# Kernel tuning notes

Hardware: AMD Instinct MI355X
Metric: run time of the kernel (lower is better)

Reference implementation:

```python
import jax, jax.numpy as jnp
import numpy as np

C = 384          # hardcoded input dim in Head
H = 6            # num_heads
D = 64           # head_size (H*D == C)

def setup_inputs() -> dict:
    key = jax.random.key(0)
    ks = jax.random.split(key, 6)
    x = jax.random.normal(ks[0], (4, 2048, C), dtype=jnp.float32)
    # per-head projection weights stacked: [H, C, D]
    s = 1.0 / np.sqrt(C)
    Wq = jax.random.uniform(ks[1], (H, C, D), minval=-s, maxval=s, dtype=jnp.float32)
    Wk = jax.random.uniform(ks[2], (H, C, D), minval=-s, maxval=s, dtype=jnp.float32)
    Wv = jax.random.uniform(ks[3], (H, C, D), minval=-s, maxval=s, dtype=jnp.float32)
    sp = 1.0 / np.sqrt(H * D)
    Wo = jax.random.uniform(ks[4], (H * D, H * D), minval=-sp, maxval=sp, dtype=jnp.float32)
    bo = jax.random.uniform(ks[5], (H * D,), minval=-sp, maxval=sp, dtype=jnp.float32)
    return {"x": x, "Wq": Wq, "Wk": Wk, "Wv": Wv, "Wo": Wo, "bo": bo}

def reference(x, Wq, Wk, Wv, Wo, bo):
    B, T, _ = x.shape
    # per-head projections (batched over heads instead of a Python loop)
    q = jnp.einsum('btc,hcd->bhtd', x, Wq)
    k = jnp.einsum('btc,hcd->bhtd', x, Wk)
    v = jnp.einsum('btc,hcd->bhtd', x, Wv)
    scale = 1.0 / jnp.sqrt(jnp.asarray(D, dtype=x.dtype))
    scores = jnp.einsum('bhtd,bhsd->bhts', q, k) * scale  # [B,H,T,T]
    attn = jax.nn.softmax(scores, axis=-1)                # no causal mask in source
    out = jnp.einsum('bhts,bhsd->bhtd', attn, v)          # [B,H,T,D]
    # concat heads: [B,T,H*D] (head order matches torch.cat over heads)
    out = out.transpose(0, 2, 1, 3).reshape(B, T, H * D)
    return out @ Wo + bo
```

## Files before the change

### kernel.cpp

```cpp
#include <hip/hip_runtime.h>

typedef unsigned short u16;
typedef float  f32x4 __attribute__((ext_vector_type(4)));
typedef short  s16x8 __attribute__((ext_vector_type(8)));
typedef unsigned int u32x2 __attribute__((ext_vector_type(2)));
typedef unsigned int u32x4 __attribute__((ext_vector_type(4)));

union U8 { u32x4 u; u32x2 u2[2]; s16x8 s; unsigned int uw[4]; };

__device__ __forceinline__ u16 f2bs(float f) {
    union { float f; unsigned int u; } x; x.f = f;
    return (u16)((x.u + 0x7FFFu + ((x.u >> 16) & 1u)) >> 16);
}

__device__ __forceinline__ unsigned int cvtpk(float a, float b) {
    unsigned int r;
    asm("v_cvt_pk_bf16_f32 %0, %1, %2" : "=v"(r) : "v"(a), "v"(b));
    return r;
}

#if __has_builtin(__builtin_amdgcn_exp2f)
#define EXP2(v) __builtin_amdgcn_exp2f(v)
#else
#define EXP2(v) exp2f(v)
#endif

__device__ __forceinline__ f32x4 mfma16(s16x8 a, s16x8 b, f32x4 c) {
    return __builtin_amdgcn_mfma_f32_16x16x32_bf16(a, b, c, 0, 0, 0);
}

typedef __attribute__((address_space(3))) unsigned int lds_u32;
typedef const __attribute__((address_space(1))) unsigned int glb_u32;
__device__ __forceinline__ void gl16(const u16* g, u16* l) {
    __builtin_amdgcn_global_load_lds((glb_u32*)g, (lds_u32*)l, 16, 0, 0);
}

__global__ __launch_bounds__(256) void pack_w2(const float* __restrict__ Wq,
                                               const float* __restrict__ Wk,
                                               const float* __restrict__ Wv,
                                               const float* __restrict__ Wo,
                                               u16* __restrict__ Wt) {
    __shared__ float tile[64][65];
    const int bid = blockIdx.x, tid = threadIdx.x;
    const float* src; u16* dst; int src_ld, sr0, sc0;
    if (bid < 108) {
        int tensor = bid / 36, rem = bid % 36, h = rem / 6, ct = rem % 6;
        const float* W = (tensor == 0) ? Wq : (tensor == 1) ? Wk : Wv;
        src = W + h * 24576; src_ld = 64; sr0 = ct * 64; sc0 = 0;
        dst = Wt + tensor * 147456 + h * 24576;
    } else {
        int rem = bid - 108, et = rem / 6, ft = rem % 6;
        src = Wo; src_ld = 384; sr0 = ft * 64; sc0 = et * 64;
        dst = Wt + 3 * 147456;
    }
    const int r = tid >> 2, cb = (tid & 3) * 16;
    const float* sp = src + (size_t)(sr0 + r) * src_ld + sc0 + cb;
    #pragma unroll
    for (int j = 0; j < 4; ++j)
        *(f32x4*)&tile[r][cb + j * 4] = *(const f32x4*)(sp + j * 4);
    __syncthreads();
    struct alignas(16) OV { u16 v[16]; } ov;
    #pragma unroll
    for (int j = 0; j < 16; ++j) ov.v[j] = f2bs(tile[cb + j][r]);
    u16* dp = dst + (size_t)(sc0 + r) * 384 + sr0 + cb;
    *(u32x4*)dp       = *(u32x4*)&ov.v[0];
    *(u32x4*)(dp + 8) = *(u32x4*)&ov.v[8];
}

__global__ __launch_bounds__(256) void convert_x(const float* __restrict__ x, u16* __restrict__ xb) {
    const int i = (blockIdx.x * 256 + threadIdx.x) * 8;
    f32x4 a = *(const f32x4*)(x + i);
    f32x4 b = *(const f32x4*)(x + i + 4);
    U8 o;
    #pragma unroll
    for (int j = 0; j < 4; ++j) { o.s[j] = (short)f2bs(a[j]); o.s[4 + j] = (short)f2bs(b[j]); }
    *(u32x4*)(xb + i) = o.u;
}

__global__ __launch_bounds__(256) void proj2(const u16* __restrict__ xb,
                                             const u16* __restrict__ Wt,
                                             u16* __restrict__ Qb,
                                             u16* __restrict__ Kb,
                                             u16* __restrict__ Vb) {
    __shared__ u16 As[2][128 * 32];
    __shared__ u16 Bs[2][128 * 32];
    const int tid = threadIdx.x, w = tid >> 6, lane = tid & 63;
    const int lr = lane & 15, lg = lane >> 4;
    const int wr = w >> 1, wc = w & 1;
    const int mt = blockIdx.x, nt = blockIdx.y;
    const int m0 = mt * 128, n0 = nt * 128;

    const int c0 = w * 2 * 64 + lane;
    const int ar0 = c0 >> 2, acc0 = c0 & 3;
    const int c1 = c0 + 64;
    const int ar1 = c1 >> 2, acc1 = c1 & 3;
    const u16* gA0 = xb + (size_t)(m0 + ar0) * 384 + acc0 * 8;
    const u16* gA1 = xb + (size_t)(m0 + ar1) * 384 + acc1 * 8;
    const u16* gB0 = Wt + (size_t)(n0 + ar0) * 384 + acc0 * 8;
    const u16* gB1 = Wt + (size_t)(n0 + ar1) * 384 + acc1 * 8;

    f32x4 acc[4][4];
    #pragma unroll
    for (int i = 0; i < 4; ++i)
        #pragma unroll
        for (int j = 0; j < 4; ++j) acc[i][j] = f32x4{0.f, 0.f, 0.f, 0.f};

    gl16(gA0, &As[0][(w * 2 + 0) * 512]);
    gl16(gA1, &As[0][(w * 2 + 1) * 512]);
    gl16(gB0, &Bs[0][(w * 2 + 0) * 512]);
    gl16(gB1, &Bs[0][(w * 2 + 1) * 512]);
    __syncthreads();

    for (int kt = 0; kt < 12; ++kt) {
        const int buf = kt & 1;
        if (kt < 11) {
            const int ko = (kt + 1) * 32;
            gl16(gA0 + ko, &As[buf ^ 1][(w * 2 + 0) * 512]);
            gl16(gA1 + ko, &As[buf ^ 1][(w * 2 + 1) * 512]);
            gl16(gB0 + ko, &Bs[buf ^ 1][(w * 2 + 0) * 512]);
            gl16(gB1 + ko, &Bs[buf ^ 1][(w * 2 + 1) * 512]);
        }
        U8 af[4], bf[4];
        #pragma unroll
        for (int f = 0; f < 4; ++f) {
            af[f].u = *(const u32x4*)&As[buf][(wr * 64 + f * 16 + lr) * 32 + lg * 8];
            bf[f].u = *(const u32x4*)&Bs[buf][(wc * 64 + f * 16 + lr) * 32 + lg * 8];
        }
        #pragma unroll
        for (int mf = 0; mf < 4; ++mf)
            #pragma unroll
            for (int nf = 0; nf < 4; ++nf)
                acc[mf][nf] = mfma16(af[mf].s, bf[nf].s, acc[mf][nf]);
        __syncthreads();
    }

    const int tensor = nt / 3;
    u16* dst = (tensor == 0) ? Qb : (tensor == 1) ? Kb : Vb;
    const float scl = (tensor == 0) ? 0.18033688011112042f : 1.0f;
    const int head_base = (nt % 3) * 2 + wc;
    #pragma unroll
    for (int mf = 0; mf < 4; ++mf)
        #pragma unroll
        for (int nf = 0; nf < 4; ++nf)
            #pragma unroll
            for (int r = 0; r < 4; ++r) {
                int m = m0 + wr * 64 + mf * 16 + lg * 4 + r;
                int b = m >> 11, t = m & 2047;
                int d = nf * 16 + lr;
                dst[((size_t)(b * 6 + head_base) * 2048 + t) * 64 + d] = f2bs(acc[mf][nf][r] * scl);
            }
}

__global__ __launch_bounds__(256) void transpose_v(const u16* __restrict__ Vb,
                                                   u16* __restrict__ Vt) {
    __shared__ u16 tile[64][72];
    const int bh = blockIdx.y, t0 = blockIdx.x * 64;
    const int tid = threadIdx.x;
    const int r = tid >> 2, c0 = (tid & 3) * 16;
    const u16* src = Vb + ((size_t)bh * 2048 + t0 + r) * 64 + c0;
    u32x4 a  = *(const u32x4*)(src);
    u32x4 b2 = *(const u32x4*)(src + 8);
    *(u32x4*)&tile[r][c0]     = a;
    *(u32x4*)&tile[r][c0 + 8] = b2;
    __syncthreads();
    struct alignas(16) OutV { u16 v[16]; } ov;
    #pragma unroll
    for (int j = 0; j < 16; ++j) ov.v[j] = tile[c0 + j][r];
    u16* dst = Vt + ((size_t)bh * 64 + r) * 2048 + t0 + c0;
    *(u32x4*)dst       = *(u32x4*)&ov.v[0];
    *(u32x4*)(dst + 8) = *(u32x4*)&ov.v[8];
}

__global__ __launch_bounds__(256) void attn3(const u16* __restrict__ Qb,
                                             const u16* __restrict__ Kb,
                                             const u16* __restrict__ Vt,
                                             u16* __restrict__ AO) {
    __shared__ char smem[32768];
    const int tid = threadIdx.x, w = tid >> 6, lane = tid & 63;
    const int lr = lane & 15, lg = lane >> 4;
    const int qt = blockIdx.x, bh = blockIdx.y;
    const int b = bh / 6, h = bh - b * 6;
    const int qbase = qt * 64 + w * 16;

    const u16* qp = Qb + ((size_t)bh * 2048 + qbase + lr) * 64 + lg * 8;
    U8 bq0, bq1;
    bq0.u = *(const u32x4*)qp;
    bq1.u = *(const u32x4*)(qp + 32);

    const int srow = lane >> 3;
    const int slot = lane & 7;
    const int chunk = slot ^ srow;
    const u16* kg0 = Kb + (size_t)bh * 2048 * 64 + (size_t)(w * 16 + srow) * 64 + chunk * 8;
    const u16* kg1 = kg0 + 8 * 64;
    const u16* vg0 = Vt + (size_t)bh * 64 * 2048 + (size_t)(w * 16 + srow) * 2048 + chunk * 8;
    const u16* vg1 = vg0 + 8 * 2048;

    const int rx = lr & 7;
    const int kOffA = lr * 128 + ((lg ^ rx) * 16);
    const int kOffB = lr * 128 + (((4 + lg) ^ rx) * 16);
    const int vRow = lr * 128 + (lg & 1) * 8;
    const int vC = lg >> 1;

    f32x4 acc[4];
    #pragma unroll
    for (int i = 0; i < 4; ++i) acc[i] = f32x4{0.f, 0.f, 0.f, 0.f};
    float rsum = 0.f;

    gl16(kg0, (u16*)(smem + w * 2048));
    gl16(kg1, (u16*)(smem + w * 2048 + 1024));
    gl16(vg0, (u16*)(smem + 8192 + w * 2048));
    gl16(vg1, (u16*)(smem + 8192 + w * 2048 + 1024));
    kg0 += 4096; kg1 += 4096; vg0 += 64; vg1 += 64;
    __syncthreads();

    for (int it = 0; it < 32; ++it) {
        const int buf = it & 1;
        const char* kbase = smem + buf * 16384;
        const char* vbase = kbase + 8192;

        if (it < 31) {
            char* nb = smem + (buf ^ 1) * 16384;
            gl16(kg0, (u16*)(nb + w * 2048));
            gl16(kg1, (u16*)(nb + w * 2048 + 1024));
            gl16(vg0, (u16*)(nb + 8192 + w * 2048));
            gl16(vg1, (u16*)(nb + 8192 + w * 2048 + 1024));
            kg0 += 4096; kg1 += 4096; vg0 += 64; vg1 += 64;
        }

        float p[16];
        const f32x4 z{0.f, 0.f, 0.f, 0.f};
        #pragma unroll
        for (int t = 0; t < 4; ++t) {
            U8 ak0, ak1;
            ak0.u = *(const u32x4*)(kbase + t * 2048 + kOffA);
            ak1.u = *(const u32x4*)(kbase + t * 2048 + kOffB);
            f32x4 s = mfma16(ak0.s, bq0.s, z);
            s = mfma16(ak1.s, bq1.s, s);
            #pragma unroll
            for (int r = 0; r < 4; ++r) p[t * 4 + r] = EXP2(s[r]);
        }
        #pragma unroll
        for (int i = 0; i < 16; ++i) rsum += p[i];

        U8 pa0, pa1;
        #pragma unroll
        for (int i = 0; i < 4; ++i) {
            pa0.uw[i] = cvtpk(p[2 * i],     p[2 * i + 1]);
            pa1.uw[i] = cvtpk(p[8 + 2 * i], p[9 + 2 * i]);
        }

        #pragma unroll
        for (int dt = 0; dt < 4; ++dt) {
            const char* vr = vbase + dt * 2048 + vRow;
            U8 bv0, bv1;
            bv0.u2[0] = *(const u32x2*)(vr + (((0 + vC) ^ rx) << 4));
            bv0.u2[1] = *(const u32x2*)(vr + (((2 + vC) ^ rx) << 4));
            bv1.u2[0] = *(const u32x2*)(vr + (((4 + vC) ^ rx) << 4));
            bv1.u2[1] = *(const u32x2*)(vr + (((6 + vC) ^ rx) << 4));
            acc[dt] = mfma16(pa0.s, bv0.s, acc[dt]);
            acc[dt] = mfma16(pa1.s, bv1.s, acc[dt]);
        }
        __syncthreads();
    }

    rsum += __shfl_xor(rsum, 16, 64);
    rsum += __shfl_xor(rsum, 32, 64);

    const size_t aobase = ((size_t)b * 2048 + qbase) * 384 + h * 64;
    #pragma unroll
    for (int r = 0; r < 4; ++r) {
        float inv = 1.0f / __shfl(rsum, lg * 4 + r, 64);
        #pragma unroll
        for (int dt = 0; dt < 4; ++dt)
            AO[aobase + (size_t)(lg * 4 + r) * 384 + dt * 16 + lr] = f2bs(acc[dt][r] * inv);
    }
}

__global__ __launch_bounds__(256) void outproj2(const u16* __restrict__ AO,
                                                const u16* __restrict__ Wot,
                                                const float* __restrict__ bo,
                                                float* __restrict__ out) {
    __shared__ u16 As[2][64 * 32];
    __shared__ u16 Bs[2][64 * 32];
    const int tid = threadIdx.x, w = tid >> 6, lane = tid & 63;
    const int lr = lane & 15, lg = lane >> 4;
    const int wr = w >> 1, wc = w & 1;
    const int mt = blockIdx.x, nt = blockIdx.y;
    const int m0 = mt * 64, n0 = nt * 64;

    const int c0 = w * 64 + lane;
    const int ar0 = c0 >> 2, cc0 = c0 & 3;
    const u16* gA = AO  + (size_t)(m0 + ar0) * 384 + cc0 * 8;
    const u16* gB = Wot + (size_t)(n0 + ar0) * 384 + cc0 * 8;

    f32x4 acc[2][2];
    #pragma unroll
    for (int i = 0; i < 2; ++i)
        #pragma unroll
        for (int j = 0; j < 2; ++j) acc[i][j] = f32x4{0.f, 0.f, 0.f, 0.f};

    gl16(gA, &As[0][w * 512]);
    gl16(gB, &Bs[0][w * 512]);
    __syncthreads();

    for (int kt = 0; kt < 12; ++kt) {
        const int buf = kt & 1;
        if (kt < 11) {
            const int ko = (kt + 1) * 32;
            gl16(gA + ko, &As[buf ^ 1][w * 512]);
            gl16(gB + ko, &Bs[buf ^ 1][w * 512]);
        }
        U8 af[2], bf[2];
        #pragma unroll
        for (int f = 0; f < 2; ++f) {
            af[f].u = *(const u32x4*)&As[buf][(wr * 32 + f * 16 + lr) * 32 + lg * 8];
            bf[f].u = *(const u32x4*)&Bs[buf][(wc * 32 + f * 16 + lr) * 32 + lg * 8];
        }
        #pragma unroll
        for (int mf = 0; mf < 2; ++mf)
            #pragma unroll
            for (int nf = 0; nf < 2; ++nf)
                acc[mf][nf] = mfma16(af[mf].s, bf[nf].s, acc[mf][nf]);
        __syncthreads();
    }

    #pragma unroll
    for (int mf = 0; mf < 2; ++mf)
        #pragma unroll
        for (int nf = 0; nf < 2; ++nf) {
            int col = n0 + wc * 32 + nf * 16 + lr;
            float bias = bo[col];
            #pragma unroll
            for (int r = 0; r < 4; ++r) {
                int m = m0 + wr * 32 + mf * 16 + lg * 4 + r;
                out[(size_t)m * 384 + col] = acc[mf][nf][r] + bias;
            }
        }
}

extern "C" void kernel_launch(void* const* d_in, const int* in_sizes, int n_in,
                              void* d_out, int out_size, void* d_ws, size_t ws_size,
                              hipStream_t stream) {
    const float* x  = (const float*)d_in[0];
    const float* Wq = (const float*)d_in[1];
    const float* Wk = (const float*)d_in[2];
    const float* Wv = (const float*)d_in[3];
    const float* Wo = (const float*)d_in[4];
    const float* bo = (const float*)d_in[5];
    float* out = (float*)d_out;
    char* ws = (char*)d_ws;

    u16* Wt  = (u16*)(ws);
    u16* Wot = (u16*)(ws + 884736);
    u16* xb  = (u16*)(ws + 1179648);
    u16* Qb  = (u16*)(ws + 7471104);
    u16* Kb  = (u16*)(ws + 13762560);
    u16* Vb  = (u16*)(ws + 20054016);
    u16* Vt  = (u16*)(ws + 26345472);
    u16* AO  = (u16*)(ws + 1179648);

    pack_w2<<<144, 256, 0, stream>>>(Wq, Wk, Wv, Wo, Wt);
    convert_x<<<1536, 256, 0, stream>>>(x, xb);
    proj2<<<dim3(64, 9), 256, 0, stream>>>(xb, Wt, Qb, Kb, Vb);
    transpose_v<<<dim3(32, 24), 256, 0, stream>>>(Vb, Vt);
    attn3<<<dim3(32, 24), 256, 0, stream>>>(Qb, Kb, Vt, AO);
    outproj2<<<dim3(128, 6), 256, 0, stream>>>(AO, Wot, bo, out);
}
```

Baseline: 145.9 us.

## Rewrite attention with 32x32 MFMA tiles and split-KV across wave pairs

Replaces the 16x16x32 MFMA attention kernel with one using 32x32x16 bf16 MFMAs. Each pair of waves shares a 32-query tile and splits the key range in half, and the partial outputs and row sums are merged through shared memory at the end. The V transpose kernel now permutes its column order to match the new operand layout. The aim is fewer, larger matrix instructions and fewer LDS operand reads per FLOP, at the cost of a final cross-wave reduction and higher accumulator register pressure.

```diff
diff --git a/kernel.cpp b/kernel.cpp
--- a/kernel.cpp
+++ b/kernel.cpp
@@ -1,8 +1,9 @@
 #include <hip/hip_runtime.h>
 
 typedef unsigned short u16;
-typedef float  f32x4 __attribute__((ext_vector_type(4)));
-typedef short  s16x8 __attribute__((ext_vector_type(8)));
+typedef float  f32x4  __attribute__((ext_vector_type(4)));
+typedef float  f32x16 __attribute__((ext_vector_type(16)));
+typedef short  s16x8  __attribute__((ext_vector_type(8)));
 typedef unsigned int u32x2 __attribute__((ext_vector_type(2)));
 typedef unsigned int u32x4 __attribute__((ext_vector_type(4)));
 
@@ -27,6 +28,9 @@
 
 __device__ __forceinline__ f32x4 mfma16(s16x8 a, s16x8 b, f32x4 c) {
     return __builtin_amdgcn_mfma_f32_16x16x32_bf16(a, b, c, 0, 0, 0);
+}
+__device__ __forceinline__ f32x16 mfma32(s16x8 a, s16x8 b, f32x16 c) {
+    return __builtin_amdgcn_mfma_f32_32x32x16_bf16(a, b, c, 0, 0, 0);
 }
 
 typedef __attribute__((address_space(3))) unsigned int lds_u32;
@@ -165,114 +169,143 @@
     __syncthreads();
     struct alignas(16) OutV { u16 v[16]; } ov;
     #pragma unroll
-    for (int j = 0; j < 16; ++j) ov.v[j] = tile[c0 + j][r];
+    for (int j = 0; j < 4; ++j) {
+        ov.v[j]      = tile[c0 + j][r];
+        ov.v[4 + j]  = tile[c0 + 8 + j][r];
+        ov.v[8 + j]  = tile[c0 + 4 + j][r];
+        ov.v[12 + j] = tile[c0 + 12 + j][r];
+    }
     u16* dst = Vt + ((size_t)bh * 64 + r) * 2048 + t0 + c0;
     *(u32x4*)dst       = *(u32x4*)&ov.v[0];
     *(u32x4*)(dst + 8) = *(u32x4*)&ov.v[8];
 }
 
-__global__ __launch_bounds__(256) void attn3(const u16* __restrict__ Qb,
+__global__ __launch_bounds__(256) void attn4(const u16* __restrict__ Qb,
                                              const u16* __restrict__ Kb,
                                              const u16* __restrict__ Vt,
                                              u16* __restrict__ AO) {
     __shared__ char smem[32768];
-    const int tid = threadIdx.x, w = tid >> 6, lane = tid & 63;
-    const int lr = lane & 15, lg = lane >> 4;
+    const int tid = threadIdx.x, wv = tid >> 6, lane = tid & 63;
+    const int qs = wv >> 1, kh = wv & 1;
+    const int q = lane & 31, hi = lane >> 5;
     const int qt = blockIdx.x, bh = blockIdx.y;
     const int b = bh / 6, h = bh - b * 6;
-    const int qbase = qt * 64 + w * 16;
-
-    const u16* qp = Qb + ((size_t)bh * 2048 + qbase + lr) * 64 + lg * 8;
-    U8 bq0, bq1;
-    bq0.u = *(const u32x4*)qp;
-    bq1.u = *(const u32x4*)(qp + 32);
-
-    const int srow = lane >> 3;
-    const int slot = lane & 7;
-    const int chunk = slot ^ srow;
-    const u16* kg0 = Kb + (size_t)bh * 2048 * 64 + (size_t)(w * 16 + srow) * 64 + chunk * 8;
-    const u16* kg1 = kg0 + 8 * 64;
-    const u16* vg0 = Vt + (size_t)bh * 64 * 2048 + (size_t)(w * 16 + srow) * 2048 + chunk * 8;
-    const u16* vg1 = vg0 + 8 * 2048;
-
-    const int rx = lr & 7;
-    const int kOffA = lr * 128 + ((lg ^ rx) * 16);
-    const int kOffB = lr * 128 + (((4 + lg) ^ rx) * 16);
-    const int vRow = lr * 128 + (lg & 1) * 8;
-    const int vC = lg >> 1;
-
-    f32x4 acc[4];
-    #pragma unroll
-    for (int i = 0; i < 4; ++i) acc[i] = f32x4{0.f, 0.f, 0.f, 0.f};
+    const int qbase = qt * 64 + qs * 32;
+
+    const u16* qp = Qb + ((size_t)bh * 2048 + qbase + q) * 64 + hi * 8;
+    U8 bq[4];
+    #pragma unroll
+    for (int m = 0; m < 4; ++m) bq[m].u = *(const u32x4*)(qp + m * 16);
+
+    const int l8 = lane >> 3, c8 = lane & 7;
+    const int kr = qs * 16 + l8;
+    const u16* ksrc = Kb + ((size_t)bh * 2048 + kh * 1024 + kr) * 64 + ((c8 ^ (kr & 7)) * 8);
+    const int kdst = kh * 4096 + qs * 2048;
+    const int lv4 = lane >> 2, c4 = lane & 3;
+    const int vr = qs * 32 + lv4;
+    const u16* vsrc = Vt + ((size_t)bh * 64 + vr) * 2048 + kh * 1024 + ((c4 ^ (vr & 3)) * 8);
+    const int vdst = 8192 + kh * 4096 + qs * 2048;
+
+    int koff[4], voff[2];
+    #pragma unroll
+    for (int m = 0; m < 4; ++m)
+        koff[m] = kh * 4096 + q * 128 + (((2 * m + hi) ^ (q & 7)) << 4);
+    #pragma unroll
+    for (int kg = 0; kg < 2; ++kg)
+        voff[kg] = 8192 + kh * 4096 + q * 64 + (((2 * kg + hi) ^ (q & 3)) << 4);
+
+    f32x16 acc[2];
+    #pragma unroll
+    for (int i = 0; i < 2; ++i)
+        #pragma unroll
+        for (int r = 0; r < 16; ++r) acc[i][r] = 0.f;
     float rsum = 0.f;
 
-    gl16(kg0, (u16*)(smem + w * 2048));
-    gl16(kg1, (u16*)(smem + w * 2048 + 1024));
-    gl16(vg0, (u16*)(smem + 8192 + w * 2048));
-    gl16(vg1, (u16*)(smem + 8192 + w * 2048 + 1024));
-    kg0 += 4096; kg1 += 4096; vg0 += 64; vg1 += 64;
-    __syncthreads();
-
+    gl16(ksrc,         (u16*)(smem + kdst));
+    gl16(ksrc + 512,   (u16*)(smem + kdst + 1024));
+    gl16(vsrc,         (u16*)(smem + vdst));
+    gl16(vsrc + 32768, (u16*)(smem + vdst + 1024));
+    ksrc += 2048; vsrc += 32;
+    __syncthreads();
+
+    #pragma unroll 2
     for (int it = 0; it < 32; ++it) {
         const int buf = it & 1;
-        const char* kbase = smem + buf * 16384;
-        const char* vbase = kbase + 8192;
-
+        const char* bsm = smem + buf * 16384;
         if (it < 31) {
-            char* nb = smem + (buf ^ 1) * 16384;
-            gl16(kg0, (u16*)(nb + w * 2048));
-            gl16(kg1, (u16*)(nb + w * 2048 + 1024));
-            gl16(vg0, (u16*)(nb + 8192 + w * 2048));
-            gl16(vg1, (u16*)(nb + 8192 + w * 2048 + 1024));
-            kg0 += 4096; kg1 += 4096; vg0 += 64; vg1 += 64;
+            char* nsm = smem + (buf ^ 1) * 16384;
+            gl16(ksrc,         (u16*)(nsm + kdst));
+            gl16(ksrc + 512,   (u16*)(nsm + kdst + 1024));
+            gl16(vsrc,         (u16*)(nsm + vdst));
+            gl16(vsrc + 32768, (u16*)(nsm + vdst + 1024));
+            ksrc += 2048; vsrc += 32;
+        }
+
+        f32x16 S;
+        #pragma unroll
+        for (int r = 0; r < 16; ++r) S[r] = 0.f;
+        #pragma unroll
+        for (int m = 0; m < 4; ++m) {
+            U8 ak; ak.u = *(const u32x4*)(bsm + koff[m]);
+            S = mfma32(ak.s, bq[m].s, S);
         }
 
         float p[16];
-        const f32x4 z{0.f, 0.f, 0.f, 0.f};
-        #pragma unroll
-        for (int t = 0; t < 4; ++t) {
-            U8 ak0, ak1;
-            ak0.u = *(const u32x4*)(kbase + t * 2048 + kOffA);
-            ak1.u = *(const u32x4*)(kbase + t * 2048 + kOffB);
-            f32x4 s = mfma16(ak0.s, bq0.s, z);
-            s = mfma16(ak1.s, bq1.s, s);
-            #pragma unroll
-            for (int r = 0; r < 4; ++r) p[t * 4 + r] = EXP2(s[r]);
-        }
-        #pragma unroll
-        for (int i = 0; i < 16; ++i) rsum += p[i];
-
-        U8 pa0, pa1;
+        #pragma unroll
+        for (int r = 0; r < 16; ++r) p[r] = EXP2(S[r]);
+        float t0 = (p[0] + p[1]) + (p[2] + p[3]);
+        float t1 = (p[4] + p[5]) + (p[6] + p[7]);
+        float t2 = (p[8] + p[9]) + (p[10] + p[11]);
+        float t3 = (p[12] + p[13]) + (p[14] + p[15]);
+        rsum += (t0 + t1) + (t2 + t3);
+
+        U8 paA, paB;
         #pragma unroll
         for (int i = 0; i < 4; ++i) {
-            pa0.uw[i] = cvtpk(p[2 * i],     p[2 * i + 1]);
-            pa1.uw[i] = cvtpk(p[8 + 2 * i], p[9 + 2 * i]);
-        }
-
-        #pragma unroll
-        for (int dt = 0; dt < 4; ++dt) {
-            const char* vr = vbase + dt * 2048 + vRow;
+            paA.uw[i] = cvtpk(p[2 * i],     p[2 * i + 1]);
+            paB.uw[i] = cvtpk(p[8 + 2 * i], p[9 + 2 * i]);
+        }
+
+        #pragma unroll
+        for (int dt2 = 0; dt2 < 2; ++dt2) {
             U8 bv0, bv1;
-            bv0.u2[0] = *(const u32x2*)(vr + (((0 + vC) ^ rx) << 4));
-            bv0.u2[1] = *(const u32x2*)(vr + (((2 + vC) ^ rx) << 4));
-            bv1.u2[0] = *(const u32x2*)(vr + (((4 + vC) ^ rx) << 4));
-            bv1.u2[1] = *(const u32x2*)(vr + (((6 + vC) ^ rx) << 4));
-            acc[dt] = mfma16(pa0.s, bv0.s, acc[dt]);
-            acc[dt] = mfma16(pa1.s, bv1.s, acc[dt]);
+            bv0.u = *(const u32x4*)(bsm + voff[0] + dt2 * 2048);
+            bv1.u = *(const u32x4*)(bsm + voff[1] + dt2 * 2048);
+            acc[dt2] = mfma32(paA.s, bv0.s, acc[dt2]);
+            acc[dt2] = mfma32(paB.s, bv1.s, acc[dt2]);
         }
         __syncthreads();
     }
 
-    rsum += __shfl_xor(rsum, 16, 64);
-    rsum += __shfl_xor(rsum, 32, 64);
-
-    const size_t aobase = ((size_t)b * 2048 + qbase) * 384 + h * 64;
-    #pragma unroll
-    for (int r = 0; r < 4; ++r) {
-        float inv = 1.0f / __shfl(rsum, lg * 4 + r, 64);
-        #pragma unroll
-        for (int dt = 0; dt < 4; ++dt)
-            AO[aobase + (size_t)(lg * 4 + r) * 384 + dt * 16 + lr] = f2bs(acc[dt][r] * inv);
+    float rsum2 = rsum + __shfl_xor(rsum, 32, 64);
+
+    float* mbase = (float*)smem + qs * 2176;
+    if (kh == 1) {
+        #pragma unroll
+        for (int dt2 = 0; dt2 < 2; ++dt2)
+            #pragma unroll
+            for (int r = 0; r < 16; ++r)
+                mbase[(dt2 * 16 + r) * 64 + lane] = acc[dt2][r];
+        mbase[2048 + lane] = rsum2;
+    }
+    __syncthreads();
+    if (kh == 0) {
+        #pragma unroll
+        for (int dt2 = 0; dt2 < 2; ++dt2)
+            #pragma unroll
+            for (int r = 0; r < 16; ++r)
+                acc[dt2][r] += mbase[(dt2 * 16 + r) * 64 + lane];
+        float rtot = rsum2 + mbase[2048 + lane];
+        float inv = 1.0f / rtot;
+        const size_t aobase = ((size_t)b * 2048 + qbase) * 384 + h * 64;
+        #pragma unroll
+        for (int r = 0; r < 16; ++r) {
+            const int qrow = (r & 3) + 8 * (r >> 2) + 4 * hi;
+            float vinv = __shfl(inv, qrow, 64);
+            #pragma unroll
+            for (int dt2 = 0; dt2 < 2; ++dt2)
+                AO[aobase + (size_t)qrow * 384 + dt2 * 32 + q] = f2bs(acc[dt2][r] * vinv);
+        }
     }
 }
 
@@ -363,6 +396,6 @@
     convert_x<<<1536, 256, 0, stream>>>(x, xb);
     proj2<<<dim3(64, 9), 256, 0, stream>>>(xb, Wt, Qb, Kb, Vb);
     transpose_v<<<dim3(32, 24), 256, 0, stream>>>(Vb, Vt);
-    attn3<<<dim3(32, 24), 256, 0, stream>>>(Qb, Kb, Vt, AO);
+    attn4<<<dim3(32, 24), 256, 0, stream>>>(Qb, Kb, Vt, AO);
     outproj2<<<dim3(128, 6), 256, 0, stream>>>(AO, Wot, bo, out);
 }
```

Result: faster. 139.8 us (-4.2%).
